# Kernel optimization log

Hardware: AMD Instinct MI355X
Metric: run time of the kernel (lower is better)

## Reference

```python
import jax, jax.numpy as jnp
import numpy as np

B, S, D_IN = 4, 2048, 1024
EMBED, H = 1024, 16
HD = EMBED // H  # 64


def setup_inputs() -> dict:
    key = jax.random.key(0)
    k1, k2, k3 = jax.random.split(key, 3)
    x = jax.random.normal(k1, (B, S, D_IN), dtype=jnp.float32)
    # xavier_uniform for torch Linear weight [out, in]
    lim_qkv = float(np.sqrt(6.0 / (D_IN + 3 * EMBED)))
    W_qkv = jax.random.uniform(k2, (3 * EMBED, D_IN), minval=-lim_qkv, maxval=lim_qkv, dtype=jnp.float32)
    b_qkv = jnp.zeros((3 * EMBED,), dtype=jnp.float32)
    lim_o = float(np.sqrt(6.0 / (EMBED + EMBED)))
    W_out = jax.random.uniform(k3, (EMBED, EMBED), minval=-lim_o, maxval=lim_o, dtype=jnp.float32)
    b_out = jnp.zeros((EMBED,), dtype=jnp.float32)
    return {"x": x, "W_qkv": W_qkv, "b_qkv": b_qkv, "W_out": W_out, "b_out": b_out}


def reference(x, W_qkv, b_qkv, W_out, b_out):
    b, s, _ = x.shape
    qkv = x @ W_qkv.T + b_qkv                      # [b, s, 3*embed]
    # einops 'b s (h c d) -> c b h s d': fused dim groups as (h, 3, d)
    qkv = qkv.reshape(b, s, H, 3, HD)
    qkv = jnp.transpose(qkv, (3, 0, 2, 1, 4))      # [3, b, h, s, d]
    q, k, v = qkv[0], qkv[1], qkv[2]
    scale = 1.0 / jnp.sqrt(jnp.asarray(HD, dtype=q.dtype))
    logits = jnp.einsum('bhqd,bhkd->bhqk', q, k) * scale
    attn = jax.nn.softmax(logits, axis=-1)
    vals = jnp.einsum('bhqk,bhkd->bhqd', attn, v)  # [b, h, s, d]
    vals = jnp.transpose(vals, (0, 2, 1, 3)).reshape(b, s, EMBED)
    return vals @ W_out.T + b_out
```

## Files before the change

kernel.cpp:

```cpp
#include <hip/hip_runtime.h>
#include <hip/hip_bf16.h>
#include <stdint.h>

#define B_   4
#define S_   2048
#define DIN  1024
#define EMB  1024
#define H_   16
#define HD_  64
#define TOK  (B_*S_)
#define NQKV 3072

using bf16  = __hip_bfloat16;
using f32x4 = __attribute__((ext_vector_type(4))) float;
using f32x16 = __attribute__((ext_vector_type(16))) float;
using s16x8 = __attribute__((ext_vector_type(8))) short;
using bf16x8 = __attribute__((ext_vector_type(8))) __bf16;

__device__ __forceinline__ f32x4 mfma16(s16x8 a, s16x8 b, f32x4 c) {
  return __builtin_amdgcn_mfma_f32_16x16x32_bf16(
      __builtin_bit_cast(bf16x8, a), __builtin_bit_cast(bf16x8, b), c, 0, 0, 0);
}
__device__ __forceinline__ f32x16 mfma32(s16x8 a, s16x8 b, f32x16 c) {
  return __builtin_amdgcn_mfma_f32_32x32x16_bf16(
      __builtin_bit_cast(bf16x8, a), __builtin_bit_cast(bf16x8, b), c, 0, 0, 0);
}

__device__ __forceinline__ void gload_lds16(const void* g, void* l) {
  __builtin_amdgcn_global_load_lds(
      (const __attribute__((address_space(1))) uint32_t*)g,
      (__attribute__((address_space(3))) uint32_t*)l, 16, 0, 0);
}

__device__ __forceinline__ uint32_t cvtpk_bf16(float lo, float hi) {
  uint32_t r;
  asm("v_cvt_pk_bf16_f32 %0, %1, %2" : "=v"(r) : "v"(lo), "v"(hi));
  return r;
}
__device__ __forceinline__ void plswap32(uint32_t &a, uint32_t &b) {
  asm("v_permlane32_swap_b32 %0, %1" : "+v"(a), "+v"(b));
}

union U8 { s16x8 v; bf16 b[8]; };
union PaU { uint32_t w[4]; s16x8 v; };

__global__ __launch_bounds__(256) void cvt_bf16(const float* __restrict__ in,
                                                bf16* __restrict__ out, int n) {
  int i = (blockIdx.x * 256 + threadIdx.x) * 8;
  if (i >= n) return;
  float4 a = *(const float4*)(in + i);
  float4 b = *(const float4*)(in + i + 4);
  U8 u;
  u.b[0] = __float2bfloat16(a.x); u.b[1] = __float2bfloat16(a.y);
  u.b[2] = __float2bfloat16(a.z); u.b[3] = __float2bfloat16(a.w);
  u.b[4] = __float2bfloat16(b.x); u.b[5] = __float2bfloat16(b.y);
  u.b[6] = __float2bfloat16(b.z); u.b[7] = __float2bfloat16(b.w);
  *(s16x8*)(out + i) = u.v;
}

template<int MODE>
__global__ __launch_bounds__(256) void gemm_bt(
    const bf16* __restrict__ A, const bf16* __restrict__ Bw,
    const float* __restrict__ bias,
    bf16* __restrict__ outQK, bf16* __restrict__ outV,
    float* __restrict__ outF, int N, int K)
{
  const int tid  = threadIdx.x;
  const int lane = tid & 63;
  const int w    = tid >> 6;
  const int wm   = w >> 1, wn = w & 1;
  const int bn0  = blockIdx.x * 128;
  const int bm0  = blockIdx.y * 128;

  __shared__ __align__(16) bf16 As[128 * 64];
  __shared__ __align__(16) bf16 Bs[128 * 64];

  f32x4 acc[4][4];
  const f32x4 zero = {0.f, 0.f, 0.f, 0.f};
  for (int mt = 0; mt < 4; ++mt)
    for (int nt = 0; nt < 4; ++nt) acc[mt][nt] = zero;

  for (int kt = 0; kt < K; kt += 64) {
    for (int i = 0; i < 4; ++i) {
      int c   = i * 256 + tid;
      int row = c >> 3, p = c & 7;
      int sc  = p ^ (row & 7);
      gload_lds16(A + (size_t)(bm0 + row) * K + kt + sc * 8, (char*)As + c * 16);
      gload_lds16(Bw + (size_t)(bn0 + row) * K + kt + sc * 8, (char*)Bs + c * 16);
    }
    __syncthreads();

    s16x8 af[4][2], bfr[4][2];
    for (int mt = 0; mt < 4; ++mt)
      for (int kk = 0; kk < 2; ++kk) {
        int row  = wm * 64 + mt * 16 + (lane & 15);
        int byte = row * 128 + (((kk * 4 + (lane >> 4)) ^ (row & 7)) << 4);
        af[mt][kk] = *(const s16x8*)((const char*)As + byte);
      }
    for (int nt = 0; nt < 4; ++nt)
      for (int kk = 0; kk < 2; ++kk) {
        int row  = wn * 64 + nt * 16 + (lane & 15);
        int byte = row * 128 + (((kk * 4 + (lane >> 4)) ^ (row & 7)) << 4);
        bfr[nt][kk] = *(const s16x8*)((const char*)Bs + byte);
      }
    for (int kk = 0; kk < 2; ++kk)
      for (int mt = 0; mt < 4; ++mt)
        for (int nt = 0; nt < 4; ++nt)
          acc[mt][nt] = mfma16(af[mt][kk], bfr[nt][kk], acc[mt][nt]);
    __syncthreads();
  }

  const int col_l = lane & 15;
  const int rgrp  = lane >> 4;
  for (int mt = 0; mt < 4; ++mt)
    for (int nt = 0; nt < 4; ++nt) {
      int n0  = bn0 + wn * 64 + nt * 16;
      int col = n0 + col_l;
      float bv = bias[col];
      if (MODE == 0) {
        int h = col / 192, rem = col % 192;
        int cc = rem / 64, d = rem % 64;
        for (int r = 0; r < 4; ++r) {
          int row = bm0 + wm * 64 + mt * 16 + rgrp * 4 + r;
          bf16 bvv = __float2bfloat16(acc[mt][nt][r] + bv);
          if (cc == 2) {
            int bb = row >> 11, s = row & 2047;
            outV[(((size_t)bb * H_ + h) * HD_ + d) * S_ + s] = bvv;
          } else {
            outQK[(size_t)row * NQKV + col] = bvv;
          }
        }
      } else {
        for (int r = 0; r < 4; ++r) {
          int row = bm0 + wm * 64 + mt * 16 + rgrp * 4 + r;
          outF[(size_t)row * EMB + col] = acc[mt][nt][r] + bv;
        }
      }
    }
}

__global__ __launch_bounds__(512) void attn2(const bf16* __restrict__ qkvb,
                                             const bf16* __restrict__ vb,
                                             bf16* __restrict__ ob)
{
  const int tid = threadIdx.x, lane = tid & 63, w = tid >> 6;
  const int hi = lane >> 5, l31 = lane & 31;
  const int f  = blockIdx.x;
  const int bh = (f & 7) | (((f >> 6) & 7) << 3);
  const int qt = (f >> 3) & 7;
  const int bb = bh >> 4, h = bh & 15;
  const int q0 = qt * 256;
  const size_t tokbase = (size_t)bb * S_;

  __shared__ __align__(16) bf16 Ks[2][64 * 64];
  __shared__ __align__(16) bf16 Vts[2][64 * 64];

  s16x8 qf[4];
  {
    const int qrow = q0 + w * 32 + l31;
    const bf16* qp = qkvb + (tokbase + qrow) * NQKV + h * 192 + hi * 8;
    #pragma unroll
    for (int ks = 0; ks < 4; ++ks) {
      U8 u; u.v = *(const s16x8*)(qp + ks * 16);
      #pragma unroll
      for (int j = 0; j < 8; ++j)
        u.b[j] = __float2bfloat16(__bfloat162float(u.b[j]) * 0.18033688011112042f);
      qf[ks] = u.v;
    }
  }

  f32x16 zero16;
  #pragma unroll
  for (int i = 0; i < 16; ++i) zero16[i] = 0.f;
  f32x16 oA = zero16, oB = zero16;
  f32x16 nm16 = zero16;
  float l0 = 0.f;

  const bf16* Kbase = qkvb + tokbase * NQKV + h * 192 + 64;
  const bf16* Vbase = vb + (size_t)bh * HD_ * S_;

  auto STAGE = [&](int b, int t) {
    const int kv0 = t * 64;
    const int c = tid;
    const int row = c >> 3, p = c & 7, sc = p ^ (row & 7);
    gload_lds16(Kbase + (size_t)(kv0 + row) * NQKV + sc * 8,
                (char*)Ks[b] + c * 16);
    gload_lds16(Vbase + (size_t)row * S_ + kv0 + sc * 8,
                (char*)Vts[b] + c * 16);
  };

  STAGE(0, 0);
  __syncthreads();

  int cur = 0;
  for (int t = 0; t < S_ / 64; ++t) {
    if (t < S_ / 64 - 1) STAGE(cur ^ 1, t + 1);

    f32x16 pA, pB;
    #pragma unroll
    for (int ks = 0; ks < 4; ++ks) {
      {
        int arow = l31;
        int byte = arow * 128 + (((2 * ks + hi) ^ (arow & 7)) << 4);
        s16x8 kf = *(const s16x8*)((const char*)Ks[cur] + byte);
        pA = mfma32(kf, qf[ks], ks == 0 ? nm16 : pA);
      }
      {
        int arow = 32 + l31;
        int byte = arow * 128 + (((2 * ks + hi) ^ (arow & 7)) << 4);
        s16x8 kf = *(const s16x8*)((const char*)Ks[cur] + byte);
        pB = mfma32(kf, qf[ks], ks == 0 ? nm16 : pB);
      }
    }

    float mx8[8];
    #pragma unroll
    for (int i = 0; i < 8; ++i)
      mx8[i] = fmaxf(fmaxf(pA[i], pA[i + 8]), fmaxf(pB[i], pB[i + 8]));
    float pmax = fmaxf(fmaxf(fmaxf(mx8[0], mx8[4]), fmaxf(mx8[1], mx8[5])),
                       fmaxf(fmaxf(mx8[2], mx8[6]), fmaxf(mx8[3], mx8[7])));
    pmax = fmaxf(pmax, __shfl_xor(pmax, 32));

    if (__any(pmax > 11.0f)) {
      float al = __builtin_amdgcn_exp2f(-pmax);
      l0 *= al;
      #pragma unroll
      for (int r = 0; r < 16; ++r) {
        float alr = __shfl(al, (r & 3) + 8 * (r >> 2) + 4 * hi);
        oA[r] *= alr; oB[r] *= alr;
      }
      #pragma unroll
      for (int r = 0; r < 16; ++r) { pA[r] -= pmax; pB[r] -= pmax; }
      #pragma unroll
      for (int i = 0; i < 16; ++i) nm16[i] -= pmax;
    }

    #pragma unroll
    for (int r = 0; r < 16; ++r) {
      pA[r] = __builtin_amdgcn_exp2f(pA[r]);
      pB[r] = __builtin_amdgcn_exp2f(pB[r]);
    }
    float s8[8];
    #pragma unroll
    for (int i = 0; i < 8; ++i)
      s8[i] = (pA[i] + pA[i + 8]) + (pB[i] + pB[i + 8]);
    l0 += ((s8[0] + s8[1]) + (s8[2] + s8[3])) +
          ((s8[4] + s8[5]) + (s8[6] + s8[7]));

    #pragma unroll
    for (int s = 0; s < 4; ++s) {
      const int sub = s & 1;
      const f32x16 &ph = (s < 2) ? pA : pB;
      uint32_t L0 = cvtpk_bf16(ph[8 * sub + 0], ph[8 * sub + 1]);
      uint32_t L1 = cvtpk_bf16(ph[8 * sub + 2], ph[8 * sub + 3]);
      uint32_t H0 = cvtpk_bf16(ph[8 * sub + 4], ph[8 * sub + 5]);
      uint32_t H1 = cvtpk_bf16(ph[8 * sub + 6], ph[8 * sub + 7]);
      plswap32(L0, H0);
      plswap32(L1, H1);
      PaU pa; pa.w[0] = L0; pa.w[1] = L1; pa.w[2] = H0; pa.w[3] = H1;
      {
        int vrow = l31;
        int byte = vrow * 128 + (((2 * s + hi) ^ (vrow & 7)) << 4);
        s16x8 vf = *(const s16x8*)((const char*)Vts[cur] + byte);
        oA = mfma32(pa.v, vf, oA);
      }
      {
        int vrow = 32 + l31;
        int byte = vrow * 128 + (((2 * s + hi) ^ (vrow & 7)) << 4);
        s16x8 vf = *(const s16x8*)((const char*)Vts[cur] + byte);
        oB = mfma32(pa.v, vf, oB);
      }
    }
    __syncthreads();
    cur ^= 1;
  }

  float l0t = l0 + __shfl_xor(l0, 32);
  float inv = 1.0f / l0t;
  #pragma unroll
  for (int r = 0; r < 16; ++r) {
    int q = (r & 3) + 8 * (r >> 2) + 4 * hi;
    float invr = __shfl(inv, q);
    int qrow = q0 + w * 32 + q;
    bf16* op = ob + (tokbase + qrow) * EMB + h * 64 + l31;
    op[0]  = __float2bfloat16(oA[r] * invr);
    op[32] = __float2bfloat16(oB[r] * invr);
  }
}

extern "C" void kernel_launch(void* const* d_in, const int* in_sizes, int n_in,
                              void* d_out, int out_size, void* d_ws, size_t ws_size,
                              hipStream_t stream) {
  const float* x    = (const float*)d_in[0];
  const float* Wqkv = (const float*)d_in[1];
  const float* bqkv = (const float*)d_in[2];
  const float* Wout = (const float*)d_in[3];
  const float* bout = (const float*)d_in[4];
  float* out = (float*)d_out;

  char* ws = (char*)d_ws;
  bf16* xb    = (bf16*)(ws);
  bf16* wqkvb = (bf16*)(ws + 16777216);
  bf16* woutb = (bf16*)(ws + 23068672);
  bf16* qkvb  = (bf16*)(ws + 25165824);
  bf16* vb    = (bf16*)(ws + 75497472);
  bf16* ob    = xb;

  cvt_bf16<<<(TOK * DIN / 8 + 255) / 256, 256, 0, stream>>>(x, xb, TOK * DIN);
  cvt_bf16<<<(NQKV * DIN / 8 + 255) / 256, 256, 0, stream>>>(Wqkv, wqkvb, NQKV * DIN);
  cvt_bf16<<<(EMB * EMB / 8 + 255) / 256, 256, 0, stream>>>(Wout, woutb, EMB * EMB);

  gemm_bt<0><<<dim3(NQKV / 128, TOK / 128), 256, 0, stream>>>(
      xb, wqkvb, bqkv, qkvb, vb, nullptr, NQKV, DIN);

  attn2<<<dim3(512), 512, 0, stream>>>(qkvb, vb, ob);

  gemm_bt<1><<<dim3(EMB / 128, TOK / 128), 256, 0, stream>>>(
      ob, woutb, bout, nullptr, nullptr, out, EMB, EMB);
}
```

Measured before the change: 222.2 us.

## Double attention KV tile to 128, fuse conversion kernels, add occupancy hint

The attention kernel now stages 128 keys/values per iteration instead of 64. That halves the loop trip count and the barriers per key, and amortises the online-softmax max/rescale over twice as many scores. The three fp32-to-bf16 conversion launches are merged into one kernel that picks its source by block index, which removes two launches. The attention kernel also gets a min-blocks hint of 4 in launch_bounds. Shared memory doubles and register pressure rises from four 32x32 score accumulators, which could cause spills under the occupancy hint.

```diff
diff --git a/kernel.cpp b/kernel.cpp
--- a/kernel.cpp
+++ b/kernel.cpp
@@ -44,17 +44,25 @@
 union U8 { s16x8 v; bf16 b[8]; };
 union PaU { uint32_t w[4]; s16x8 v; };
 
-__global__ __launch_bounds__(256) void cvt_bf16(const float* __restrict__ in,
-                                                bf16* __restrict__ out, int n) {
-  int i = (blockIdx.x * 256 + threadIdx.x) * 8;
-  if (i >= n) return;
+__global__ __launch_bounds__(256) void cvt_all(const float* __restrict__ x,
+                                               const float* __restrict__ wqkv,
+                                               const float* __restrict__ wout,
+                                               bf16* __restrict__ xb,
+                                               bf16* __restrict__ wqkvb,
+                                               bf16* __restrict__ woutb) {
+  int b = blockIdx.x;
+  const float* in; bf16* out; int base;
+  if (b < 4096)      { in = x;    out = xb;    base = b; }
+  else if (b < 5632) { in = wqkv; out = wqkvb; base = b - 4096; }
+  else               { in = wout; out = woutb; base = b - 5632; }
+  int i = (base * 256 + (int)threadIdx.x) * 8;
   float4 a = *(const float4*)(in + i);
-  float4 b = *(const float4*)(in + i + 4);
+  float4 c = *(const float4*)(in + i + 4);
   U8 u;
   u.b[0] = __float2bfloat16(a.x); u.b[1] = __float2bfloat16(a.y);
   u.b[2] = __float2bfloat16(a.z); u.b[3] = __float2bfloat16(a.w);
-  u.b[4] = __float2bfloat16(b.x); u.b[5] = __float2bfloat16(b.y);
-  u.b[6] = __float2bfloat16(b.z); u.b[7] = __float2bfloat16(b.w);
+  u.b[4] = __float2bfloat16(c.x); u.b[5] = __float2bfloat16(c.y);
+  u.b[6] = __float2bfloat16(c.z); u.b[7] = __float2bfloat16(c.w);
   *(s16x8*)(out + i) = u.v;
 }
 
@@ -139,9 +147,9 @@
     }
 }
 
-__global__ __launch_bounds__(512) void attn2(const bf16* __restrict__ qkvb,
-                                             const bf16* __restrict__ vb,
-                                             bf16* __restrict__ ob)
+__global__ __launch_bounds__(512, 4) void attn2(const bf16* __restrict__ qkvb,
+                                                const bf16* __restrict__ vb,
+                                                bf16* __restrict__ ob)
 {
   const int tid = threadIdx.x, lane = tid & 63, w = tid >> 6;
   const int hi = lane >> 5, l31 = lane & 31;
@@ -152,8 +160,8 @@
   const int q0 = qt * 256;
   const size_t tokbase = (size_t)bb * S_;
 
-  __shared__ __align__(16) bf16 Ks[2][64 * 64];
-  __shared__ __align__(16) bf16 Vts[2][64 * 64];
+  __shared__ __align__(16) bf16 Ks[2][128 * 64];
+  __shared__ __align__(16) bf16 Vts[2][64 * 128];
 
   s16x8 qf[4];
   {
@@ -180,23 +188,31 @@
   const bf16* Vbase = vb + (size_t)bh * HD_ * S_;
 
   auto STAGE = [&](int b, int t) {
-    const int kv0 = t * 64;
-    const int c = tid;
-    const int row = c >> 3, p = c & 7, sc = p ^ (row & 7);
-    gload_lds16(Kbase + (size_t)(kv0 + row) * NQKV + sc * 8,
-                (char*)Ks[b] + c * 16);
-    gload_lds16(Vbase + (size_t)row * S_ + kv0 + sc * 8,
-                (char*)Vts[b] + c * 16);
+    const int kv0 = t * 128;
+    #pragma unroll
+    for (int i = 0; i < 2; ++i) {
+      int c = i * 512 + tid;
+      int row = c >> 3, p = c & 7, sc = p ^ (row & 7);
+      gload_lds16(Kbase + (size_t)(kv0 + row) * NQKV + sc * 8,
+                  (char*)Ks[b] + c * 16);
+    }
+    #pragma unroll
+    for (int i = 0; i < 2; ++i) {
+      int c = i * 512 + tid;
+      int row = c >> 4, p = c & 15, sc = p ^ (row & 7);
+      gload_lds16(Vbase + (size_t)row * S_ + kv0 + sc * 8,
+                  (char*)Vts[b] + c * 16);
+    }
   };
 
   STAGE(0, 0);
   __syncthreads();
 
   int cur = 0;
-  for (int t = 0; t < S_ / 64; ++t) {
-    if (t < S_ / 64 - 1) STAGE(cur ^ 1, t + 1);
-
-    f32x16 pA, pB;
+  for (int t = 0; t < S_ / 128; ++t) {
+    if (t < S_ / 128 - 1) STAGE(cur ^ 1, t + 1);
+
+    f32x16 pA, pB, pC, pD;
     #pragma unroll
     for (int ks = 0; ks < 4; ++ks) {
       {
@@ -211,12 +227,25 @@
         s16x8 kf = *(const s16x8*)((const char*)Ks[cur] + byte);
         pB = mfma32(kf, qf[ks], ks == 0 ? nm16 : pB);
       }
+      {
+        int arow = 64 + l31;
+        int byte = arow * 128 + (((2 * ks + hi) ^ (arow & 7)) << 4);
+        s16x8 kf = *(const s16x8*)((const char*)Ks[cur] + byte);
+        pC = mfma32(kf, qf[ks], ks == 0 ? nm16 : pC);
+      }
+      {
+        int arow = 96 + l31;
+        int byte = arow * 128 + (((2 * ks + hi) ^ (arow & 7)) << 4);
+        s16x8 kf = *(const s16x8*)((const char*)Ks[cur] + byte);
+        pD = mfma32(kf, qf[ks], ks == 0 ? nm16 : pD);
+      }
     }
 
     float mx8[8];
     #pragma unroll
     for (int i = 0; i < 8; ++i)
-      mx8[i] = fmaxf(fmaxf(pA[i], pA[i + 8]), fmaxf(pB[i], pB[i + 8]));
+      mx8[i] = fmaxf(fmaxf(fmaxf(pA[i], pA[i + 8]), fmaxf(pB[i], pB[i + 8])),
+                     fmaxf(fmaxf(pC[i], pC[i + 8]), fmaxf(pD[i], pD[i + 8])));
     float pmax = fmaxf(fmaxf(fmaxf(mx8[0], mx8[4]), fmaxf(mx8[1], mx8[5])),
                        fmaxf(fmaxf(mx8[2], mx8[6]), fmaxf(mx8[3], mx8[7])));
     pmax = fmaxf(pmax, __shfl_xor(pmax, 32));
@@ -230,7 +259,9 @@
         oA[r] *= alr; oB[r] *= alr;
       }
       #pragma unroll
-      for (int r = 0; r < 16; ++r) { pA[r] -= pmax; pB[r] -= pmax; }
+      for (int r = 0; r < 16; ++r) {
+        pA[r] -= pmax; pB[r] -= pmax; pC[r] -= pmax; pD[r] -= pmax;
+      }
       #pragma unroll
       for (int i = 0; i < 16; ++i) nm16[i] -= pmax;
     }
@@ -239,36 +270,43 @@
     for (int r = 0; r < 16; ++r) {
       pA[r] = __builtin_amdgcn_exp2f(pA[r]);
       pB[r] = __builtin_amdgcn_exp2f(pB[r]);
+      pC[r] = __builtin_amdgcn_exp2f(pC[r]);
+      pD[r] = __builtin_amdgcn_exp2f(pD[r]);
     }
     float s8[8];
     #pragma unroll
     for (int i = 0; i < 8; ++i)
-      s8[i] = (pA[i] + pA[i + 8]) + (pB[i] + pB[i + 8]);
+      s8[i] = ((pA[i] + pA[i + 8]) + (pB[i] + pB[i + 8])) +
+              ((pC[i] + pC[i + 8]) + (pD[i] + pD[i + 8]));
     l0 += ((s8[0] + s8[1]) + (s8[2] + s8[3])) +
           ((s8[4] + s8[5]) + (s8[6] + s8[7]));
 
     #pragma unroll
-    for (int s = 0; s < 4; ++s) {
-      const int sub = s & 1;
-      const f32x16 &ph = (s < 2) ? pA : pB;
-      uint32_t L0 = cvtpk_bf16(ph[8 * sub + 0], ph[8 * sub + 1]);
-      uint32_t L1 = cvtpk_bf16(ph[8 * sub + 2], ph[8 * sub + 3]);
-      uint32_t H0 = cvtpk_bf16(ph[8 * sub + 4], ph[8 * sub + 5]);
-      uint32_t H1 = cvtpk_bf16(ph[8 * sub + 6], ph[8 * sub + 7]);
-      plswap32(L0, H0);
-      plswap32(L1, H1);
-      PaU pa; pa.w[0] = L0; pa.w[1] = L1; pa.w[2] = H0; pa.w[3] = H1;
-      {
-        int vrow = l31;
-        int byte = vrow * 128 + (((2 * s + hi) ^ (vrow & 7)) << 4);
-        s16x8 vf = *(const s16x8*)((const char*)Vts[cur] + byte);
-        oA = mfma32(pa.v, vf, oA);
-      }
-      {
-        int vrow = 32 + l31;
-        int byte = vrow * 128 + (((2 * s + hi) ^ (vrow & 7)) << 4);
-        s16x8 vf = *(const s16x8*)((const char*)Vts[cur] + byte);
-        oB = mfma32(pa.v, vf, oB);
+    for (int h2 = 0; h2 < 2; ++h2) {
+      #pragma unroll
+      for (int s = 0; s < 4; ++s) {
+        const int sub = s & 1;
+        const f32x16 &ph = h2 ? ((s < 2) ? pC : pD) : ((s < 2) ? pA : pB);
+        uint32_t L0 = cvtpk_bf16(ph[8 * sub + 0], ph[8 * sub + 1]);
+        uint32_t L1 = cvtpk_bf16(ph[8 * sub + 2], ph[8 * sub + 3]);
+        uint32_t H0 = cvtpk_bf16(ph[8 * sub + 4], ph[8 * sub + 5]);
+        uint32_t H1 = cvtpk_bf16(ph[8 * sub + 6], ph[8 * sub + 7]);
+        plswap32(L0, H0);
+        plswap32(L1, H1);
+        PaU pa; pa.w[0] = L0; pa.w[1] = L1; pa.w[2] = H0; pa.w[3] = H1;
+        const int ch = 8 * h2 + 2 * s + hi;
+        {
+          int vrow = l31;
+          int byte = vrow * 256 + ((ch ^ (vrow & 7)) << 4);
+          s16x8 vf = *(const s16x8*)((const char*)Vts[cur] + byte);
+          oA = mfma32(pa.v, vf, oA);
+        }
+        {
+          int vrow = 32 + l31;
+          int byte = vrow * 256 + ((ch ^ (vrow & 7)) << 4);
+          s16x8 vf = *(const s16x8*)((const char*)Vts[cur] + byte);
+          oB = mfma32(pa.v, vf, oB);
+        }
       }
     }
     __syncthreads();
@@ -306,9 +344,7 @@
   bf16* vb    = (bf16*)(ws + 75497472);
   bf16* ob    = xb;
 
-  cvt_bf16<<<(TOK * DIN / 8 + 255) / 256, 256, 0, stream>>>(x, xb, TOK * DIN);
-  cvt_bf16<<<(NQKV * DIN / 8 + 255) / 256, 256, 0, stream>>>(Wqkv, wqkvb, NQKV * DIN);
-  cvt_bf16<<<(EMB * EMB / 8 + 255) / 256, 256, 0, stream>>>(Wout, woutb, EMB * EMB);
+  cvt_all<<<dim3(6144), 256, 0, stream>>>(x, Wqkv, Wout, xb, wqkvb, woutb);
 
   gemm_bt<0><<<dim3(NQKV / 128, TOK / 128), 256, 0, stream>>>(
       xb, wqkvb, bqkv, qkvb, vb, nullptr, NQKV, DIN);
```

New measurement: 534.2 us. 140% more time.
